# Kernel tuning notes

Hardware: AMD Instinct MI355X
Metric: run time of the kernel (lower is better)

Reference implementation:

```python
import jax, jax.numpy as jnp
import numpy as np

NHEADS = 16

def setup_inputs() -> dict:
    key = jax.random.key(0)
    ks = jax.random.split(key, 5)
    C = 1024
    d = C // NHEADS
    x  = jax.random.normal(ks[0], (2, 2048, C), dtype=jnp.float32)
    sc = 1.0 / np.sqrt(C)
    wq = jax.random.normal(ks[1], (C, C), dtype=jnp.float32) * sc
    wk = jax.random.normal(ks[2], (C, C), dtype=jnp.float32) * sc
    wv = jax.random.normal(ks[3], (C, C), dtype=jnp.float32) * sc
    wo = jax.random.normal(ks[4], (d, C), dtype=jnp.float32) * (1.0 / np.sqrt(d))
    return {"x": x, "wq": wq, "wk": wk, "wv": wv, "wo": wo}

def reference(x, wq, wk, wv, wo):
    B, T, C = x.shape
    H = NHEADS
    d = C // H

    def split_heads(y):
        return y.reshape(B, T, H, d).transpose(0, 2, 1, 3)  # [B,H,T,d]

    Q = split_heads(x @ wq)
    K = split_heads(x @ wk)
    V = split_heads(x @ wv)

    # scores[b,h,q,k]
    prod = jnp.einsum('bhqd,bhkd->bhqk', Q, K) / np.sqrt(d)

    # ALiBi bias: offset[h, q, k] = (k - q) * 2**(-8*(h+1)/H)
    idx = jnp.arange(T)
    slopes = jnp.exp2(-8.0 * (jnp.arange(H, dtype=jnp.float32) + 1.0) / H)
    bias = (idx[None, :] - idx[:, None]).astype(x.dtype) * slopes[:, None, None]
    prod = prod + bias[None]

    # causal tril mask: keep k <= q
    keep = idx[None, :] <= idx[:, None]  # [T_q, T_k]
    prod = jnp.where(keep[None, None], prod, -jnp.inf)

    # NOTE: original uses F.softmax(prod, 2) -> softmax over the QUERY axis.
    attention_weights = jax.nn.softmax(prod, axis=2)
    attention_output = jnp.einsum('bhqk,bhkd->bhqd', attention_weights, V)

    # per-head wo projection then sum over heads == (sum over heads) @ wo (linear)
    outputs = attention_output.sum(axis=1) @ wo  # [B,T,C]
    return x + outputs
```

## Files before the change

kernel.cpp:

```cpp
#include <hip/hip_runtime.h>
#include <math.h>

#define NB 2
#define NH 16
#define NT 2048
#define ND 64
#define NC 1024
#define L2E 1.44269504f

typedef __attribute__((ext_vector_type(4))) float f32x4;
typedef __attribute__((ext_vector_type(8))) short short8;
typedef __attribute__((ext_vector_type(4))) short short4_t;
typedef __attribute__((ext_vector_type(8))) unsigned short ushort8;
typedef __attribute__((ext_vector_type(4))) unsigned short ushort4_t;

__device__ const int WTAB[16] = {2,2,3,3,4,5,6,8,11,15,21,29,32,32,32,32};

#define GLOAD_LDS(gp, lp)                                                \
    __builtin_amdgcn_global_load_lds(                                    \
        (const __attribute__((address_space(1))) void*)(gp),             \
        (__attribute__((address_space(3))) void*)(lp), 16, 0, 0)

__device__ __forceinline__ int sigma_p(int p) {
    return 4 * ((p >> 3) & 3) + (p & 3) + 16 * ((p >> 2) & 1) + 32 * (p >> 5);
}

__device__ __forceinline__ unsigned short f2bf(float f) {
    unsigned u = __builtin_bit_cast(unsigned, f);
    unsigned r = (u + 0x7FFFu + ((u >> 16) & 1u)) >> 16;
    return (unsigned short)r;
}

__device__ __forceinline__ float bf2f(unsigned short s) {
    return __builtin_bit_cast(float, (unsigned)s << 16);
}

__device__ __forceinline__ unsigned cvtpk_bf16(float lo, float hi) {
    unsigned r;
    asm("v_cvt_pk_bf16_f32 %0, %1, %2" : "=v"(r) : "v"(lo), "v"(hi));
    return r;
}

__device__ __forceinline__ f32x4 mfma16(short8 a, short8 b, f32x4 c) {
    return __builtin_amdgcn_mfma_f32_16x16x32_bf16(a, b, c, 0, 0, 0);
}

__device__ __forceinline__ short8 frag_load(const unsigned short* rowp, int g, int half) {
    short8 v;
    short4_t lo = *(const short4_t*)(rowp + 4 * g + 32 * half);
    short4_t hi = *(const short4_t*)(rowp + 4 * g + 16 + 32 * half);
    #pragma unroll
    for (int j = 0; j < 4; ++j) { v[j] = lo[j]; v[4 + j] = hi[j]; }
    return v;
}

__device__ __forceinline__ short8 frag_g(const unsigned short* rowp, int g, int half) {
    return *(const short8*)(rowp + 8 * g + 32 * half);
}

__device__ __forceinline__ short8 frag_swz128(const unsigned short* tile, int row, int g, int half) {
    const char* p = (const char*)tile + row * 128 + (((g + 4 * half) ^ (row & 7)) << 4);
    return *(const short8*)p;
}

__device__ __forceinline__ short8 frag_swz32(const unsigned short* tile, int row, int g) {
    const char* p = (const char*)tile + row * 64 + (((g ^ ((row >> 1) & 3))) << 4);
    return *(const short8*)p;
}

__global__ __launch_bounds__(256) void cvt_x(const float* __restrict__ src,
                                             unsigned short* __restrict__ dst, int n4) {
    int i = blockIdx.x * 256 + threadIdx.x;
    if (i >= n4) return;
    const int blk = i >> 4, c4 = i & 15;
    const int gg = (c4 >> 1) & 3, bb = c4 & 1, hh = c4 >> 3;
    f32x4 v = ((const f32x4*)src)[blk * 16 + gg + 4 * bb + 8 * hh];
    ushort4_t o;
    #pragma unroll
    for (int j = 0; j < 4; ++j) o[j] = f2bf(v[j]);
    ((ushort4_t*)dst)[i] = o;
}

__global__ __launch_bounds__(256) void cvtW(const float* __restrict__ w0,
                                            const float* __restrict__ w1,
                                            const float* __restrict__ w2,
                                            const float* __restrict__ w3,
                                            unsigned short* __restrict__ Wt_all,
                                            unsigned short* __restrict__ Wot) {
    __shared__ __align__(16) float T[64][68];
    const int z = blockIdx.z;
    const int tid = threadIdx.x;
    if (z == 3) {
        if (blockIdx.x != 0) return;
        const int n0 = blockIdx.y * 64;
        #pragma unroll
        for (int p = 0; p < 4; ++p) {
            int r = 16 * p + (tid >> 4);
            int c = (tid & 15) * 4;
            *(f32x4*)&T[r][c] = *(const f32x4*)&w3[(size_t)r * NC + n0 + c];
        }
        __syncthreads();
        const int nr = tid >> 2, kc = (tid & 3) * 16;
        ushort8 o0, o1;
        #pragma unroll
        for (int j = 0; j < 8; ++j) { o0[j] = f2bf(T[kc + j][nr]); o1[j] = f2bf(T[kc + 8 + j][nr]); }
        unsigned short* q = Wot + (size_t)(n0 + nr) * ND + kc;
        *(ushort8*)q       = o0;
        *(ushort8*)(q + 8) = o1;
        return;
    }
    const float* W = (z == 0) ? w0 : ((z == 1) ? w1 : w2);
    unsigned short* Wt = Wt_all + (size_t)z * NC * NC;
    const int k0 = blockIdx.x * 64, n0 = blockIdx.y * 64;
    #pragma unroll
    for (int p = 0; p < 4; ++p) {
        int r = 16 * p + (tid >> 4);
        int c = (tid & 15) * 4;
        *(f32x4*)&T[r][c] = *(const f32x4*)&W[(size_t)(k0 + r) * NC + n0 + c];
    }
    __syncthreads();
    const int nr = tid >> 2, kc = (tid & 3) * 16;
    ushort8 o0, o1;
    #pragma unroll
    for (int j = 0; j < 8; ++j) o0[j] = f2bf(T[sigma_p(kc + j)][nr]);
    #pragma unroll
    for (int j = 0; j < 8; ++j) o1[j] = f2bf(T[sigma_p(kc + 8 + j)][nr]);
    unsigned short* q = Wt + (size_t)(n0 + nr) * NC + k0 + kc;
    *(ushort8*)q       = o0;
    *(ushort8*)(q + 8) = o1;
}

__global__ __launch_bounds__(256, 3) void gemm_qkv(const unsigned short* __restrict__ Xh,
                                                   const unsigned short* __restrict__ Wt_all,
                                                   unsigned short* __restrict__ qk_dst,
                                                   unsigned short* __restrict__ Vt) {
    __shared__ __align__(16) unsigned short Xs[3][4096];
    __shared__ __align__(16) unsigned short Ws[3][4096];
    const int tid = threadIdx.x;
    const int lane = tid & 63, w = tid >> 6;
    const int g = lane >> 4, l15 = lane & 15;
    const int wr = w >> 1, wc = w & 1;
    const int m0 = blockIdx.x * 128;
    const int which = blockIdx.y >> 3;
    const int n0 = (blockIdx.y & 7) * 128;
    const unsigned short* Wt = Wt_all + (size_t)which * NC * NC;

    const int sr[2] = { (0 * 256 + w * 64 + lane) >> 2, (1 * 256 + w * 64 + lane) >> 2 };
    const int sc[2] = { ((0 * 256 + w * 64 + lane) & 3) ^ ((sr[0] >> 1) & 3),
                        ((1 * 256 + w * 64 + lane) & 3) ^ ((sr[1] >> 1) & 3) };

    f32x4 acc[4][4] = {};

    auto stage = [&](int buf, int kt) {
        const size_t kb = (size_t)kt * 64;
        #pragma unroll
        for (int i = 0; i < 2; ++i) {
            const char* xs = (const char*)Xh + (size_t)(m0 + sr[i]) * 2048 + kb + (sc[i] << 4);
            GLOAD_LDS(xs, (char*)&Xs[buf][(i * 256 + w * 64) * 8]);
            const char* ws = (const char*)Wt + (size_t)(n0 + sr[i]) * 2048 + kb + (sc[i] << 4);
            GLOAD_LDS(ws, (char*)&Ws[buf][(i * 256 + w * 64) * 8]);
        }
    };

    stage(0, 0);
    stage(1, 1);
    int cur = 0, nxt = 2;

    for (int kt = 0; kt < 32; ++kt) {
        if (kt < 31) asm volatile("s_waitcnt vmcnt(4)" ::: "memory");
        else         asm volatile("s_waitcnt vmcnt(0)" ::: "memory");
        __builtin_amdgcn_s_barrier();
        if (kt + 2 < 32) stage(nxt, kt + 2);
        short8 a[4], b[4];
        #pragma unroll
        for (int mr = 0; mr < 4; ++mr)
            a[mr] = frag_swz32(Xs[cur], 64 * wr + 16 * mr + l15, g);
        #pragma unroll
        for (int nc = 0; nc < 4; ++nc)
            b[nc] = frag_swz32(Ws[cur], 64 * wc + 16 * nc + l15, g);
        __builtin_amdgcn_s_setprio(1);
        #pragma unroll
        for (int mr = 0; mr < 4; ++mr)
            #pragma unroll
            for (int nc = 0; nc < 4; ++nc)
                acc[mr][nc] = mfma16(a[mr], b[nc], acc[mr][nc]);
        __builtin_amdgcn_s_setprio(0);
        cur = (cur == 2) ? 0 : cur + 1;
        nxt = (nxt == 2) ? 0 : nxt + 1;
    }

    if (which < 2) {
        unsigned short* dst = qk_dst + (size_t)which * (NB * NH * NT * ND);
        #pragma unroll
        for (int mr = 0; mr < 4; ++mr) {
            #pragma unroll
            for (int nc = 0; nc < 4; ++nc) {
                const int n = n0 + 64 * wc + 16 * nc + l15;
                const int hh = n >> 6;
                const int dd = 32 * (nc >> 1) + 8 * (l15 >> 2) + 4 * (nc & 1) + (l15 & 3);
                #pragma unroll
                for (int r = 0; r < 4; ++r) {
                    const int m = m0 + 64 * wr + 16 * mr + 4 * g + r;
                    const int bb = m >> 11, tt = m & (NT - 1);
                    dst[(((size_t)bb * NH + hh) * NT + tt) * ND + dd] = f2bf(acc[mr][nc][r]);
                }
            }
        }
    } else {
        #pragma unroll
        for (int mr = 0; mr < 4; ++mr) {
            const int m = m0 + 64 * wr + 16 * mr + 4 * g;
            const int bb = m >> 11, tt = m & (NT - 1);
            const int tbase = (tt & ~63) + 32 * (mr >> 1) + 8 * g + 4 * (mr & 1);
            #pragma unroll
            for (int nc = 0; nc < 4; ++nc) {
                const int n = n0 + 64 * wc + 16 * nc + l15;
                const int hh = n >> 6, dd = n & 63;
                ushort4_t o;
                #pragma unroll
                for (int r = 0; r < 4; ++r) o[r] = f2bf(acc[mr][nc][r]);
                *(ushort4_t*)&Vt[(((size_t)bb * NH + hh) * ND + dd) * NT + tbase] = o;
            }
        }
    }
}

__global__ __launch_bounds__(256, 4) void colstats(const unsigned short* __restrict__ Qh,
                                                   const unsigned short* __restrict__ Kh,
                                                   unsigned short* __restrict__ Vt) {
    __shared__ __align__(16) unsigned short Qs[3][4096];
    __shared__ __align__(16) float Ssum[64];
    const int tid = threadIdx.x;
    const int lane = tid & 63, w = tid >> 6;
    const int g = lane >> 4, l15 = lane & 15;
    const int subrow = lane >> 3;
    const int src_off = (((lane & 7) ^ subrow) << 4);
    const int lin = blockIdx.x + 32 * blockIdx.y;
    const int xcd = lin & 7, idx = lin >> 3;
    const int slot = idx & 3;
    const int j = idx >> 2;
    const int hh = (slot & 1) ? (15 - xcd) : xcd;
    const int bh = ((slot >> 1) << 4) + hh;
    const float slL2 = exp2f(-0.5f * (float)(hh + 1)) * L2E;
    const float C1 = 0.125f * L2E;
    const float s16 = 16.f * slL2;
    const int Wt = WTAB[hh];
    const int qtend = min(32, j + Wt);

    const unsigned short* kr = Kh + ((size_t)bh * NT + 64 * j + 16 * w + l15) * ND;
    const short8 ak0 = frag_g(kr, g, 0), ak1 = frag_g(kr, g, 1);
    const int k0 = 64 * j + 16 * w + 4 * g;

    const char* Qbase = (const char*)(Qh + (size_t)bh * NT * ND);
    auto stage = [&](int buf, int qt) {
        const char* qs = Qbase + (size_t)(64 * qt + 16 * w + subrow) * 128 + src_off;
        char* qd = (char*)&Qs[buf][16 * w * 64];
        GLOAD_LDS(qs, qd);
        GLOAD_LDS(qs + 1024, qd + 1024);
    };

    f32x4 acc = {};
    float rs[4];
    #pragma unroll
    for (int r = 0; r < 4; ++r) rs[r] = (float)r * slL2;

    stage(0, j);
    if (j + 1 < qtend) stage(1, j + 1);
    int cur = 0, nxt = 2;

    for (int qt = j; qt < qtend; ++qt) {
        if (qt + 1 < qtend) asm volatile("s_waitcnt vmcnt(2)" ::: "memory");
        else                asm volatile("s_waitcnt vmcnt(0)" ::: "memory");
        __builtin_amdgcn_s_barrier();
        if (qt + 2 < qtend) stage(nxt, qt + 2);
        const unsigned short* tile = Qs[cur];
        short8 qf[8];
        #pragma unroll
        for (int q4 = 0; q4 < 4; ++q4) {
            qf[2 * q4]     = frag_swz128(tile, 16 * q4 + l15, g, 0);
            qf[2 * q4 + 1] = frag_swz128(tile, 16 * q4 + l15, g, 1);
        }
        float b0 = (float)(k0 - 64 * qt - l15) * slL2;
        const bool mask = (qt == j);
        #pragma unroll
        for (int q4 = 0; q4 < 4; ++q4) {
            f32x4 d = {};
            __builtin_amdgcn_s_setprio(1);
            d = mfma16(ak0, qf[2 * q4], d);
            d = mfma16(ak1, qf[2 * q4 + 1], d);
            __builtin_amdgcn_s_setprio(0);
            #pragma unroll
            for (int r = 0; r < 4; ++r) {
                float e = exp2f(fmaf(d[r], C1, b0 + rs[r]));
                if (mask && (16 * q4 + l15 < 16 * w + 4 * g + r)) e = 0.f;
                acc[r] += e;
            }
            b0 -= s16;
        }
        cur = (cur == 2) ? 0 : cur + 1;
        nxt = (nxt == 2) ? 0 : nxt + 1;
    }
    #pragma unroll
    for (int off = 1; off <= 8; off <<= 1)
        #pragma unroll
        for (int r = 0; r < 4; ++r) acc[r] += __shfl_xor(acc[r], off);
    if (l15 == 0) {
        #pragma unroll
        for (int r = 0; r < 4; ++r) Ssum[16 * w + 4 * g + r] = acc[r];
    }
    __syncthreads();

    unsigned short* Vst = Vt + (size_t)bh * ND * NT + 64 * j;
    #pragma unroll
    for (int it = 0; it < 4; ++it) {
        const int c = 256 * it + tid;
        const int d = c >> 4;
        const int tp4 = (c & 15) * 4;
        f32x4 s = *(const f32x4*)&Ssum[sigma_p(tp4)];
        unsigned short* p = Vst + (size_t)d * NT + tp4;
        ushort4_t v = *(const ushort4_t*)p;
        ushort4_t o;
        #pragma unroll
        for (int r = 0; r < 4; ++r) o[r] = f2bf(bf2f(v[r]) / s[r]);
        *(ushort4_t*)p = o;
    }
}

__global__ __launch_bounds__(256, 3) void attn_pv(const unsigned short* __restrict__ Qh,
                                                  const unsigned short* __restrict__ Kh,
                                                  const unsigned short* __restrict__ Vt,
                                                  unsigned short* __restrict__ att) {
    __shared__ __align__(16) unsigned short Ks[3][4096];
    __shared__ __align__(16) unsigned short Vs[3][4096];
    const int tid = threadIdx.x;
    const int lane = tid & 63, w = tid >> 6;
    const int g = lane >> 4, l15 = lane & 15;
    const int subrow = lane >> 3;
    const int src_off = (((lane & 7) ^ subrow) << 4);
    const int lin = blockIdx.x + 32 * blockIdx.y;
    const int xcd = lin & 7, idx = lin >> 3;
    const int slot = idx & 3;
    const int j = 31 - (idx >> 2);
    const int hh = (slot & 1) ? (15 - xcd) : xcd;
    const int bh = ((slot >> 1) << 4) + hh;
    const int bb = bh >> 4;
    const float slL2 = exp2f(-0.5f * (float)(hh + 1)) * L2E;
    const float C1 = 0.125f * L2E;
    const float s16 = 16.f * slL2;
    const int Wt = WTAB[hh];
    const int ktmin = max(0, j - Wt + 1);

    const int q = 64 * j + 16 * w + l15;
    short8 bq0, bq1;
    {
        const unsigned short* qr = Qh + ((size_t)bh * NT + q) * ND;
        bq0 = frag_g(qr, g, 0);
        bq1 = frag_g(qr, g, 1);
    }
    float rs[4];
    #pragma unroll
    for (int r = 0; r < 4; ++r) rs[r] = (float)r * slL2;

    auto stageKV = [&](int buf, int K0) {
        const char* ksrc = (const char*)Kh + (size_t)((size_t)bh * NT + K0 + 16 * w + subrow) * 128 + src_off;
        char* kdst = (char*)&Ks[buf][16 * w * 64];
        GLOAD_LDS(ksrc, kdst);
        GLOAD_LDS(ksrc + 1024, kdst + 1024);
        const char* vsrc = (const char*)Vt + ((((size_t)bh * ND + 16 * w + subrow) * NT + K0) << 1) + src_off;
        char* vdst = (char*)&Vs[buf][16 * w * 64];
        GLOAD_LDS(vsrc, vdst);
        GLOAD_LDS(vsrc + 8 * NT * 2, vdst + 1024);
    };

    stageKV(0, 64 * ktmin);
    if (ktmin < j) stageKV(1, 64 * (ktmin + 1));
    int cur = 0, nxt = 2;

    f32x4 o[4] = {};

    for (int kt = ktmin; kt <= j; ++kt) {
        if (kt < j) asm volatile("s_waitcnt vmcnt(4)" ::: "memory");
        else        asm volatile("s_waitcnt vmcnt(0)" ::: "memory");
        __builtin_amdgcn_s_barrier();
        if (kt + 2 <= j) stageKV(nxt, 64 * (kt + 2));
        const int K0 = 64 * kt;
        short8 kf[8], vf[8];
        #pragma unroll
        for (int s4 = 0; s4 < 4; ++s4) {
            kf[2 * s4]     = frag_swz128(Ks[cur], 16 * s4 + l15, g, 0);
            kf[2 * s4 + 1] = frag_swz128(Ks[cur], 16 * s4 + l15, g, 1);
            vf[2 * s4]     = frag_swz128(Vs[cur], 16 * s4 + l15, g, 0);
            vf[2 * s4 + 1] = frag_swz128(Vs[cur], 16 * s4 + l15, g, 1);
        }
        f32x4 pacc[4];
        __builtin_amdgcn_s_setprio(1);
        #pragma unroll
        for (int s4 = 0; s4 < 4; ++s4) {
            f32x4 d = {};
            d = mfma16(kf[2 * s4], bq0, d);
            d = mfma16(kf[2 * s4 + 1], bq1, d);
            pacc[s4] = d;
        }
        __builtin_amdgcn_s_setprio(0);
        union { unsigned u[4]; short8 s; } pa[2];
        float b = (float)(K0 + 4 * g - q) * slL2;
        const bool mask = (kt == j);
        #pragma unroll
        for (int s4 = 0; s4 < 4; ++s4) {
            float p[4];
            #pragma unroll
            for (int r = 0; r < 4; ++r)
                p[r] = exp2f(fmaf(pacc[s4][r], C1, b + rs[r]));
            if (mask) {
                #pragma unroll
                for (int r = 0; r < 4; ++r)
                    if (K0 + 16 * s4 + 4 * g + r > q) p[r] = 0.f;
            }
            pa[s4 >> 1].u[2 * (s4 & 1)]     = cvtpk_bf16(p[0], p[1]);
            pa[s4 >> 1].u[2 * (s4 & 1) + 1] = cvtpk_bf16(p[2], p[3]);
            b += s16;
        }
        __builtin_amdgcn_s_setprio(1);
        #pragma unroll
        for (int n = 0; n < 4; ++n) {
            o[n] = mfma16(pa[0].s, vf[2 * n], o[n]);
            o[n] = mfma16(pa[1].s, vf[2 * n + 1], o[n]);
        }
        __builtin_amdgcn_s_setprio(0);
        cur = (cur == 2) ? 0 : cur + 1;
        nxt = (nxt == 2) ? 0 : nxt + 1;
    }
    #pragma unroll
    for (int n = 0; n < 4; ++n) {
        #pragma unroll
        for (int r = 0; r < 4; ++r) {
            att[(((size_t)bb * NT + 64 * j + 16 * w + 4 * g + r) * NH + hh) * ND + 16 * n + l15] = f2bf(o[n][r]);
        }
    }
}

__global__ __launch_bounds__(256) void headsum(const unsigned short* __restrict__ att,
                                               unsigned short* __restrict__ A) {
    const int row = blockIdx.x * 16 + (threadIdx.x >> 4);
    const int d0 = (threadIdx.x & 15) * 4;
    const unsigned short* p = att + (size_t)row * (NH * ND) + d0;
    f32x4 s = {};
    #pragma unroll
    for (int h = 0; h < NH; ++h) {
        ushort4_t v = *(const ushort4_t*)(p + h * ND);
        #pragma unroll
        for (int jj = 0; jj < 4; ++jj) s[jj] += bf2f(v[jj]);
    }
    ushort4_t o;
    #pragma unroll
    for (int jj = 0; jj < 4; ++jj) o[jj] = f2bf(s[jj]);
    *(ushort4_t*)&A[(size_t)row * ND + d0] = o;
}

__global__ __launch_bounds__(256) void out_proj(const float* __restrict__ x,
                                                const unsigned short* __restrict__ A,
                                                const unsigned short* __restrict__ Wot,
                                                float* __restrict__ out) {
    const int tid = threadIdx.x;
    const int lane = tid & 63, w = tid >> 6;
    const int g = lane >> 4, l15 = lane & 15;
    const int m0 = blockIdx.x * 64, n0 = blockIdx.y * 64;

    const unsigned short* ar = A + (size_t)(m0 + 16 * w + l15) * ND;
    short8 a0 = frag_load(ar, g, 0);
    short8 a1 = frag_load(ar, g, 1);

    f32x4 acc[4] = {};
    #pragma unroll
    for (int ns = 0; ns < 4; ++ns) {
        const unsigned short* br = Wot + (size_t)(n0 + 16 * ns + l15) * ND;
        acc[ns] = mfma16(a0, frag_load(br, g, 0), acc[ns]);
        acc[ns] = mfma16(a1, frag_load(br, g, 1), acc[ns]);
    }
    #pragma unroll
    for (int ns = 0; ns < 4; ++ns) {
        #pragma unroll
        for (int r = 0; r < 4; ++r) {
            int m = m0 + 16 * w + 4 * g + r;
            int n = n0 + 16 * ns + l15;
            out[(size_t)m * NC + n] = x[(size_t)m * NC + n] + acc[ns][r];
        }
    }
}

extern "C" void kernel_launch(void* const* d_in, const int* in_sizes, int n_in,
                              void* d_out, int out_size, void* d_ws, size_t ws_size,
                              hipStream_t stream) {
    const float* x  = (const float*)d_in[0];
    const float* wq = (const float*)d_in[1];
    const float* wk = (const float*)d_in[2];
    const float* wv = (const float*)d_in[3];
    const float* wo = (const float*)d_in[4];
    float* out = (float*)d_out;

    const size_t MB = 1u << 20;
    const size_t KB = 1u << 10;
    unsigned char* w8 = (unsigned char*)d_ws;
    unsigned short* Xh  = (unsigned short*)(w8);
    unsigned short* Wta = (unsigned short*)(w8 + 8 * MB);
    unsigned short* Qh  = (unsigned short*)(w8 + 16 * MB);
    unsigned short* Kh  = (unsigned short*)(w8 + 24 * MB);
    unsigned short* Vt  = (unsigned short*)(w8 + 32 * MB);
    unsigned short* att = (unsigned short*)(w8 + 40 * MB);
    unsigned short* A   = (unsigned short*)(w8 + 48 * MB);
    unsigned short* Wot = (unsigned short*)(w8 + 48 * MB + 512 * KB);

    cvt_x<<<(NB * NT * NC) / 1024, 256, 0, stream>>>(x, Xh, (NB * NT * NC) / 4);
    cvtW<<<dim3(16, 16, 4), 256, 0, stream>>>(wq, wk, wv, wo, Wta, Wot);

    gemm_qkv<<<dim3(32, 24), 256, 0, stream>>>(Xh, Wta, Qh, Vt);

    colstats<<<dim3(32, 32), 256, 0, stream>>>(Qh, Kh, Vt);
    attn_pv<<<dim3(32, 32), 256, 0, stream>>>(Qh, Kh, Vt, att);

    headsum<<<(NB * NT) / 16, 256, 0, stream>>>(att, A);
    out_proj<<<dim3(64, 16), 256, 0, stream>>>(x, A, Wot, out);
}
```

Before: 127.1 us.

## Split colstats and attn_pv loops across two blocks by tile parity

Doubles the grid for the column-statistics and attention kernels. Each pair of blocks handles the even and odd tiles of the reduction loop. Partial column sums go to a two-slot buffer, and a new scale_v kernel combines them and normalizes V. Partial attention outputs go to two buffers that headsum adds together. This adds parallelism for long causal windows on lightly loaded heads, at the cost of an extra kernel launch, more workspace traffic, and an extra bf16 rounding of the partial outputs.

```diff
diff --git a/kernel.cpp b/kernel.cpp
--- a/kernel.cpp
+++ b/kernel.cpp
@@ -227,16 +227,17 @@
 
 __global__ __launch_bounds__(256, 4) void colstats(const unsigned short* __restrict__ Qh,
                                                    const unsigned short* __restrict__ Kh,
-                                                   unsigned short* __restrict__ Vt) {
+                                                   float* __restrict__ Lc2) {
     __shared__ __align__(16) unsigned short Qs[3][4096];
-    __shared__ __align__(16) float Ssum[64];
     const int tid = threadIdx.x;
     const int lane = tid & 63, w = tid >> 6;
     const int g = lane >> 4, l15 = lane & 15;
     const int subrow = lane >> 3;
     const int src_off = (((lane & 7) ^ subrow) << 4);
     const int lin = blockIdx.x + 32 * blockIdx.y;
-    const int xcd = lin & 7, idx = lin >> 3;
+    const int par = lin & 1;
+    const int rest = lin >> 1;
+    const int xcd = rest & 7, idx = rest >> 3;
     const int slot = idx & 3;
     const int j = idx >> 2;
     const int hh = (slot & 1) ? (15 - xcd) : xcd;
@@ -246,6 +247,7 @@
     const float s16 = 16.f * slL2;
     const int Wt = WTAB[hh];
     const int qtend = min(32, j + Wt);
+    const int qt0 = j + ((par ^ j) & 1);
 
     const unsigned short* kr = Kh + ((size_t)bh * NT + 64 * j + 16 * w + l15) * ND;
     const short8 ak0 = frag_g(kr, g, 0), ak1 = frag_g(kr, g, 1);
@@ -264,15 +266,15 @@
     #pragma unroll
     for (int r = 0; r < 4; ++r) rs[r] = (float)r * slL2;
 
-    stage(0, j);
-    if (j + 1 < qtend) stage(1, j + 1);
+    if (qt0 < qtend) stage(0, qt0);
+    if (qt0 + 2 < qtend) stage(1, qt0 + 2);
     int cur = 0, nxt = 2;
 
-    for (int qt = j; qt < qtend; ++qt) {
-        if (qt + 1 < qtend) asm volatile("s_waitcnt vmcnt(2)" ::: "memory");
+    for (int qt = qt0; qt < qtend; qt += 2) {
+        if (qt + 2 < qtend) asm volatile("s_waitcnt vmcnt(2)" ::: "memory");
         else                asm volatile("s_waitcnt vmcnt(0)" ::: "memory");
         __builtin_amdgcn_s_barrier();
-        if (qt + 2 < qtend) stage(nxt, qt + 2);
+        if (qt + 4 < qtend) stage(nxt, qt + 4);
         const unsigned short* tile = Qs[cur];
         short8 qf[8];
         #pragma unroll
@@ -305,31 +307,33 @@
         #pragma unroll
         for (int r = 0; r < 4; ++r) acc[r] += __shfl_xor(acc[r], off);
     if (l15 == 0) {
-        #pragma unroll
-        for (int r = 0; r < 4; ++r) Ssum[16 * w + 4 * g + r] = acc[r];
-    }
-    __syncthreads();
-
-    unsigned short* Vst = Vt + (size_t)bh * ND * NT + 64 * j;
-    #pragma unroll
-    for (int it = 0; it < 4; ++it) {
-        const int c = 256 * it + tid;
-        const int d = c >> 4;
-        const int tp4 = (c & 15) * 4;
-        f32x4 s = *(const f32x4*)&Ssum[sigma_p(tp4)];
-        unsigned short* p = Vst + (size_t)d * NT + tp4;
-        ushort4_t v = *(const ushort4_t*)p;
-        ushort4_t o;
-        #pragma unroll
-        for (int r = 0; r < 4; ++r) o[r] = f2bf(bf2f(v[r]) / s[r]);
-        *(ushort4_t*)p = o;
-    }
+        float* Lp = Lc2 + (size_t)(par * 32 + bh) * NT;
+        #pragma unroll
+        for (int r = 0; r < 4; ++r) Lp[k0 + r] = acc[r];
+    }
+}
+
+__global__ __launch_bounds__(256) void scale_v(const float* __restrict__ Lc2,
+                                               unsigned short* __restrict__ Vt) {
+    const int i = blockIdx.x * 256 + threadIdx.x;
+    const int bh = i >> 15;
+    const int tpos4 = (i & 511) * 4;
+    const int tlog = (tpos4 & ~63) + sigma_p(tpos4 & 63);
+    f32x4 a = *(const f32x4*)(Lc2 + (size_t)bh * NT + tlog);
+    f32x4 b = *(const f32x4*)(Lc2 + (size_t)(32 + bh) * NT + tlog);
+    ushort4_t v = ((const ushort4_t*)Vt)[i];
+    ushort4_t o;
+    #pragma unroll
+    for (int j = 0; j < 4; ++j)
+        o[j] = f2bf(bf2f(v[j]) / (a[j] + b[j]));
+    ((ushort4_t*)Vt)[i] = o;
 }
 
 __global__ __launch_bounds__(256, 3) void attn_pv(const unsigned short* __restrict__ Qh,
                                                   const unsigned short* __restrict__ Kh,
                                                   const unsigned short* __restrict__ Vt,
-                                                  unsigned short* __restrict__ att) {
+                                                  unsigned short* __restrict__ att,
+                                                  unsigned short* __restrict__ att2) {
     __shared__ __align__(16) unsigned short Ks[3][4096];
     __shared__ __align__(16) unsigned short Vs[3][4096];
     const int tid = threadIdx.x;
@@ -338,7 +342,9 @@
     const int subrow = lane >> 3;
     const int src_off = (((lane & 7) ^ subrow) << 4);
     const int lin = blockIdx.x + 32 * blockIdx.y;
-    const int xcd = lin & 7, idx = lin >> 3;
+    const int par = lin & 1;
+    const int rest = lin >> 1;
+    const int xcd = rest & 7, idx = rest >> 3;
     const int slot = idx & 3;
     const int j = 31 - (idx >> 2);
     const int hh = (slot & 1) ? (15 - xcd) : xcd;
@@ -349,6 +355,7 @@
     const float s16 = 16.f * slL2;
     const int Wt = WTAB[hh];
     const int ktmin = max(0, j - Wt + 1);
+    const int kt0 = ktmin + ((par ^ ktmin) & 1);
 
     const int q = 64 * j + 16 * w + l15;
     short8 bq0, bq1;
@@ -372,17 +379,17 @@
         GLOAD_LDS(vsrc + 8 * NT * 2, vdst + 1024);
     };
 
-    stageKV(0, 64 * ktmin);
-    if (ktmin < j) stageKV(1, 64 * (ktmin + 1));
+    if (kt0 <= j) stageKV(0, 64 * kt0);
+    if (kt0 + 2 <= j) stageKV(1, 64 * (kt0 + 2));
     int cur = 0, nxt = 2;
 
     f32x4 o[4] = {};
 
-    for (int kt = ktmin; kt <= j; ++kt) {
-        if (kt < j) asm volatile("s_waitcnt vmcnt(4)" ::: "memory");
-        else        asm volatile("s_waitcnt vmcnt(0)" ::: "memory");
+    for (int kt = kt0; kt <= j; kt += 2) {
+        if (kt + 2 <= j) asm volatile("s_waitcnt vmcnt(4)" ::: "memory");
+        else             asm volatile("s_waitcnt vmcnt(0)" ::: "memory");
         __builtin_amdgcn_s_barrier();
-        if (kt + 2 <= j) stageKV(nxt, 64 * (kt + 2));
+        if (kt + 4 <= j) stageKV(nxt, 64 * (kt + 4));
         const int K0 = 64 * kt;
         short8 kf[8], vf[8];
         #pragma unroll
@@ -430,26 +437,30 @@
         cur = (cur == 2) ? 0 : cur + 1;
         nxt = (nxt == 2) ? 0 : nxt + 1;
     }
+    unsigned short* dst = (par == 0) ? att : att2;
     #pragma unroll
     for (int n = 0; n < 4; ++n) {
         #pragma unroll
         for (int r = 0; r < 4; ++r) {
-            att[(((size_t)bb * NT + 64 * j + 16 * w + 4 * g + r) * NH + hh) * ND + 16 * n + l15] = f2bf(o[n][r]);
+            dst[(((size_t)bb * NT + 64 * j + 16 * w + 4 * g + r) * NH + hh) * ND + 16 * n + l15] = f2bf(o[n][r]);
         }
     }
 }
 
 __global__ __launch_bounds__(256) void headsum(const unsigned short* __restrict__ att,
+                                               const unsigned short* __restrict__ att2,
                                                unsigned short* __restrict__ A) {
     const int row = blockIdx.x * 16 + (threadIdx.x >> 4);
     const int d0 = (threadIdx.x & 15) * 4;
-    const unsigned short* p = att + (size_t)row * (NH * ND) + d0;
+    const unsigned short* p  = att  + (size_t)row * (NH * ND) + d0;
+    const unsigned short* p2 = att2 + (size_t)row * (NH * ND) + d0;
     f32x4 s = {};
     #pragma unroll
     for (int h = 0; h < NH; ++h) {
-        ushort4_t v = *(const ushort4_t*)(p + h * ND);
-        #pragma unroll
-        for (int jj = 0; jj < 4; ++jj) s[jj] += bf2f(v[jj]);
+        ushort4_t v  = *(const ushort4_t*)(p + h * ND);
+        ushort4_t v2 = *(const ushort4_t*)(p2 + h * ND);
+        #pragma unroll
+        for (int jj = 0; jj < 4; ++jj) s[jj] += bf2f(v[jj]) + bf2f(v2[jj]);
     }
     ushort4_t o;
     #pragma unroll
@@ -501,23 +512,26 @@
     const size_t MB = 1u << 20;
     const size_t KB = 1u << 10;
     unsigned char* w8 = (unsigned char*)d_ws;
-    unsigned short* Xh  = (unsigned short*)(w8);
-    unsigned short* Wta = (unsigned short*)(w8 + 8 * MB);
-    unsigned short* Qh  = (unsigned short*)(w8 + 16 * MB);
-    unsigned short* Kh  = (unsigned short*)(w8 + 24 * MB);
-    unsigned short* Vt  = (unsigned short*)(w8 + 32 * MB);
-    unsigned short* att = (unsigned short*)(w8 + 40 * MB);
-    unsigned short* A   = (unsigned short*)(w8 + 48 * MB);
-    unsigned short* Wot = (unsigned short*)(w8 + 48 * MB + 512 * KB);
+    unsigned short* Xh   = (unsigned short*)(w8);
+    unsigned short* Wta  = (unsigned short*)(w8 + 8 * MB);
+    unsigned short* Qh   = (unsigned short*)(w8 + 16 * MB);
+    unsigned short* Kh   = (unsigned short*)(w8 + 24 * MB);
+    unsigned short* Vt   = (unsigned short*)(w8 + 32 * MB);
+    unsigned short* att  = (unsigned short*)(w8 + 40 * MB);
+    unsigned short* att2 = (unsigned short*)(w8 + 48 * MB);
+    float*          Lc2  = (float*)(w8 + 56 * MB);
+    unsigned short* A    = (unsigned short*)(w8 + 56 * MB + 512 * KB);
+    unsigned short* Wot  = (unsigned short*)(w8 + 57 * MB);
 
     cvt_x<<<(NB * NT * NC) / 1024, 256, 0, stream>>>(x, Xh, (NB * NT * NC) / 4);
     cvtW<<<dim3(16, 16, 4), 256, 0, stream>>>(wq, wk, wv, wo, Wta, Wot);
 
     gemm_qkv<<<dim3(32, 24), 256, 0, stream>>>(Xh, Wta, Qh, Vt);
 
-    colstats<<<dim3(32, 32), 256, 0, stream>>>(Qh, Kh, Vt);
-    attn_pv<<<dim3(32, 32), 256, 0, stream>>>(Qh, Kh, Vt, att);
-
-    headsum<<<(NB * NT) / 16, 256, 0, stream>>>(att, A);
+    colstats<<<dim3(32, 64), 256, 0, stream>>>(Qh, Kh, Lc2);
+    scale_v<<<(32 * ND * NT / 4) / 256, 256, 0, stream>>>(Lc2, Vt);
+    attn_pv<<<dim3(32, 64), 256, 0, stream>>>(Qh, Kh, Vt, att, att2);
+
+    headsum<<<(NB * NT) / 16, 256, 0, stream>>>(att, att2, A);
     out_proj<<<dim3(64, 16), 256, 0, stream>>>(x, A, Wot, out);
 }
```

Result: slower. 129.7 us (+2.0%).

## Split long-window heads across two blocks to balance attention workload

Applied to the files above, without the earlier changes.

Heads 10-15 have the widest ALiBi key windows, so their attention blocks run much longer than the rest. Each such (batch, head, query tile) is now split into two blocks, each covering half the key tiles. The second half writes to a separate att2 buffer that headsum adds in. The grid grows from 1024 to 1408 blocks and the XCD-aware head mapping is replaced, trading extra partial-output traffic and a larger headsum read for better load balance.

```diff
diff --git a/kernel.cpp b/kernel.cpp
--- a/kernel.cpp
+++ b/kernel.cpp
@@ -329,7 +329,8 @@
 __global__ __launch_bounds__(256, 3) void attn_pv(const unsigned short* __restrict__ Qh,
                                                   const unsigned short* __restrict__ Kh,
                                                   const unsigned short* __restrict__ Vt,
-                                                  unsigned short* __restrict__ att) {
+                                                  unsigned short* __restrict__ att,
+                                                  unsigned short* __restrict__ att2) {
     __shared__ __align__(16) unsigned short Ks[3][4096];
     __shared__ __align__(16) unsigned short Vs[3][4096];
     const int tid = threadIdx.x;
@@ -338,17 +339,40 @@
     const int subrow = lane >> 3;
     const int src_off = (((lane & 7) ^ subrow) << 4);
     const int lin = blockIdx.x + 32 * blockIdx.y;
-    const int xcd = lin & 7, idx = lin >> 3;
-    const int slot = idx & 3;
-    const int j = 31 - (idx >> 2);
-    const int hh = (slot & 1) ? (15 - xcd) : xcd;
-    const int bh = ((slot >> 1) << 4) + hh;
+
+    int j, hh, bh, half;
+    if (lin < 768) {
+        half = (lin < 384) ? 1 : 0;
+        const int v = (lin < 384) ? lin : (lin - 384);
+        j = 31 - (v / 12);
+        const int r = v % 12;
+        hh = 10 + (r % 6);
+        bh = (r / 6) * 16 + hh;
+    } else {
+        half = -1;
+        const int v = lin - 768;
+        j = 31 - (v / 20);
+        const int r = v % 20;
+        hh = r % 10;
+        bh = (r / 10) * 16 + hh;
+    }
     const int bb = bh >> 4;
     const float slL2 = exp2f(-0.5f * (float)(hh + 1)) * L2E;
     const float C1 = 0.125f * L2E;
     const float s16 = 16.f * slL2;
     const int Wt = WTAB[hh];
     const int ktmin = max(0, j - Wt + 1);
+
+    int ktA, ktB;
+    unsigned short* dst;
+    if (half < 0) {
+        ktA = ktmin; ktB = j; dst = att;
+    } else {
+        const int range = j - ktmin + 1;
+        const int nlow = (range + 1) >> 1;
+        if (half == 0) { ktA = ktmin;        ktB = ktmin + nlow - 1; dst = att; }
+        else           { ktA = ktmin + nlow; ktB = j;                dst = att2; }
+    }
 
     const int q = 64 * j + 16 * w + l15;
     short8 bq0, bq1;
@@ -372,82 +396,92 @@
         GLOAD_LDS(vsrc + 8 * NT * 2, vdst + 1024);
     };
 
-    stageKV(0, 64 * ktmin);
-    if (ktmin < j) stageKV(1, 64 * (ktmin + 1));
-    int cur = 0, nxt = 2;
-
     f32x4 o[4] = {};
 
-    for (int kt = ktmin; kt <= j; ++kt) {
-        if (kt < j) asm volatile("s_waitcnt vmcnt(4)" ::: "memory");
-        else        asm volatile("s_waitcnt vmcnt(0)" ::: "memory");
-        __builtin_amdgcn_s_barrier();
-        if (kt + 2 <= j) stageKV(nxt, 64 * (kt + 2));
-        const int K0 = 64 * kt;
-        short8 kf[8], vf[8];
-        #pragma unroll
-        for (int s4 = 0; s4 < 4; ++s4) {
-            kf[2 * s4]     = frag_swz128(Ks[cur], 16 * s4 + l15, g, 0);
-            kf[2 * s4 + 1] = frag_swz128(Ks[cur], 16 * s4 + l15, g, 1);
-            vf[2 * s4]     = frag_swz128(Vs[cur], 16 * s4 + l15, g, 0);
-            vf[2 * s4 + 1] = frag_swz128(Vs[cur], 16 * s4 + l15, g, 1);
-        }
-        f32x4 pacc[4];
-        __builtin_amdgcn_s_setprio(1);
-        #pragma unroll
-        for (int s4 = 0; s4 < 4; ++s4) {
-            f32x4 d = {};
-            d = mfma16(kf[2 * s4], bq0, d);
-            d = mfma16(kf[2 * s4 + 1], bq1, d);
-            pacc[s4] = d;
-        }
-        __builtin_amdgcn_s_setprio(0);
-        union { unsigned u[4]; short8 s; } pa[2];
-        float b = (float)(K0 + 4 * g - q) * slL2;
-        const bool mask = (kt == j);
-        #pragma unroll
-        for (int s4 = 0; s4 < 4; ++s4) {
-            float p[4];
-            #pragma unroll
-            for (int r = 0; r < 4; ++r)
-                p[r] = exp2f(fmaf(pacc[s4][r], C1, b + rs[r]));
-            if (mask) {
+    if (ktA <= ktB) {
+        stageKV(0, 64 * ktA);
+        if (ktA < ktB) stageKV(1, 64 * (ktA + 1));
+        int cur = 0, nxt = 2;
+
+        for (int kt = ktA; kt <= ktB; ++kt) {
+            if (kt < ktB) asm volatile("s_waitcnt vmcnt(4)" ::: "memory");
+            else          asm volatile("s_waitcnt vmcnt(0)" ::: "memory");
+            __builtin_amdgcn_s_barrier();
+            if (kt + 2 <= ktB) stageKV(nxt, 64 * (kt + 2));
+            const int K0 = 64 * kt;
+            short8 kf[8], vf[8];
+            #pragma unroll
+            for (int s4 = 0; s4 < 4; ++s4) {
+                kf[2 * s4]     = frag_swz128(Ks[cur], 16 * s4 + l15, g, 0);
+                kf[2 * s4 + 1] = frag_swz128(Ks[cur], 16 * s4 + l15, g, 1);
+                vf[2 * s4]     = frag_swz128(Vs[cur], 16 * s4 + l15, g, 0);
+                vf[2 * s4 + 1] = frag_swz128(Vs[cur], 16 * s4 + l15, g, 1);
+            }
+            f32x4 pacc[4];
+            __builtin_amdgcn_s_setprio(1);
+            #pragma unroll
+            for (int s4 = 0; s4 < 4; ++s4) {
+                f32x4 d = {};
+                d = mfma16(kf[2 * s4], bq0, d);
+                d = mfma16(kf[2 * s4 + 1], bq1, d);
+                pacc[s4] = d;
+            }
+            __builtin_amdgcn_s_setprio(0);
+            union { unsigned u[4]; short8 s; } pa[2];
+            float b = (float)(K0 + 4 * g - q) * slL2;
+            const bool mask = (kt == j);
+            #pragma unroll
+            for (int s4 = 0; s4 < 4; ++s4) {
+                float p[4];
                 #pragma unroll
                 for (int r = 0; r < 4; ++r)
-                    if (K0 + 16 * s4 + 4 * g + r > q) p[r] = 0.f;
-            }
-            pa[s4 >> 1].u[2 * (s4 & 1)]     = cvtpk_bf16(p[0], p[1]);
-            pa[s4 >> 1].u[2 * (s4 & 1) + 1] = cvtpk_bf16(p[2], p[3]);
-            b += s16;
-        }
-        __builtin_amdgcn_s_setprio(1);
-        #pragma unroll
-        for (int n = 0; n < 4; ++n) {
-            o[n] = mfma16(pa[0].s, vf[2 * n], o[n]);
-            o[n] = mfma16(pa[1].s, vf[2 * n + 1], o[n]);
-        }
-        __builtin_amdgcn_s_setprio(0);
-        cur = (cur == 2) ? 0 : cur + 1;
-        nxt = (nxt == 2) ? 0 : nxt + 1;
+                    p[r] = exp2f(fmaf(pacc[s4][r], C1, b + rs[r]));
+                if (mask) {
+                    #pragma unroll
+                    for (int r = 0; r < 4; ++r)
+                        if (K0 + 16 * s4 + 4 * g + r > q) p[r] = 0.f;
+                }
+                pa[s4 >> 1].u[2 * (s4 & 1)]     = cvtpk_bf16(p[0], p[1]);
+                pa[s4 >> 1].u[2 * (s4 & 1) + 1] = cvtpk_bf16(p[2], p[3]);
+                b += s16;
+            }
+            __builtin_amdgcn_s_setprio(1);
+            #pragma unroll
+            for (int n = 0; n < 4; ++n) {
+                o[n] = mfma16(pa[0].s, vf[2 * n], o[n]);
+                o[n] = mfma16(pa[1].s, vf[2 * n + 1], o[n]);
+            }
+            __builtin_amdgcn_s_setprio(0);
+            cur = (cur == 2) ? 0 : cur + 1;
+            nxt = (nxt == 2) ? 0 : nxt + 1;
+        }
     }
     #pragma unroll
     for (int n = 0; n < 4; ++n) {
         #pragma unroll
         for (int r = 0; r < 4; ++r) {
-            att[(((size_t)bb * NT + 64 * j + 16 * w + 4 * g + r) * NH + hh) * ND + 16 * n + l15] = f2bf(o[n][r]);
+            dst[(((size_t)bb * NT + 64 * j + 16 * w + 4 * g + r) * NH + hh) * ND + 16 * n + l15] = f2bf(o[n][r]);
         }
     }
 }
 
 __global__ __launch_bounds__(256) void headsum(const unsigned short* __restrict__ att,
+                                               const unsigned short* __restrict__ att2,
                                                unsigned short* __restrict__ A) {
     const int row = blockIdx.x * 16 + (threadIdx.x >> 4);
     const int d0 = (threadIdx.x & 15) * 4;
-    const unsigned short* p = att + (size_t)row * (NH * ND) + d0;
+    const unsigned short* p  = att  + (size_t)row * (NH * ND) + d0;
+    const unsigned short* p2 = att2 + (size_t)row * (NH * ND) + d0;
     f32x4 s = {};
     #pragma unroll
     for (int h = 0; h < NH; ++h) {
         ushort4_t v = *(const ushort4_t*)(p + h * ND);
+        #pragma unroll
+        for (int jj = 0; jj < 4; ++jj) s[jj] += bf2f(v[jj]);
+    }
+    #pragma unroll
+    for (int h = 10; h < NH; ++h) {
+        ushort4_t v = *(const ushort4_t*)(p2 + h * ND);
         #pragma unroll
         for (int jj = 0; jj < 4; ++jj) s[jj] += bf2f(v[jj]);
     }
@@ -501,14 +535,15 @@
     const size_t MB = 1u << 20;
     const size_t KB = 1u << 10;
     unsigned char* w8 = (unsigned char*)d_ws;
-    unsigned short* Xh  = (unsigned short*)(w8);
-    unsigned short* Wta = (unsigned short*)(w8 + 8 * MB);
-    unsigned short* Qh  = (unsigned short*)(w8 + 16 * MB);
-    unsigned short* Kh  = (unsigned short*)(w8 + 24 * MB);
-    unsigned short* Vt  = (unsigned short*)(w8 + 32 * MB);
-    unsigned short* att = (unsigned short*)(w8 + 40 * MB);
-    unsigned short* A   = (unsigned short*)(w8 + 48 * MB);
-    unsigned short* Wot = (unsigned short*)(w8 + 48 * MB + 512 * KB);
+    unsigned short* Xh   = (unsigned short*)(w8);
+    unsigned short* Wta  = (unsigned short*)(w8 + 8 * MB);
+    unsigned short* Qh   = (unsigned short*)(w8 + 16 * MB);
+    unsigned short* Kh   = (unsigned short*)(w8 + 24 * MB);
+    unsigned short* Vt   = (unsigned short*)(w8 + 32 * MB);
+    unsigned short* att  = (unsigned short*)(w8 + 40 * MB);
+    unsigned short* att2 = (unsigned short*)(w8 + 48 * MB);
+    unsigned short* A    = (unsigned short*)(w8 + 56 * MB);
+    unsigned short* Wot  = (unsigned short*)(w8 + 56 * MB + 512 * KB);
 
     cvt_x<<<(NB * NT * NC) / 1024, 256, 0, stream>>>(x, Xh, (NB * NT * NC) / 4);
     cvtW<<<dim3(16, 16, 4), 256, 0, stream>>>(wq, wk, wv, wo, Wta, Wot);
@@ -516,8 +551,8 @@
     gemm_qkv<<<dim3(32, 24), 256, 0, stream>>>(Xh, Wta, Qh, Vt);
 
     colstats<<<dim3(32, 32), 256, 0, stream>>>(Qh, Kh, Vt);
-    attn_pv<<<dim3(32, 32), 256, 0, stream>>>(Qh, Kh, Vt, att);
-
-    headsum<<<(NB * NT) / 16, 256, 0, stream>>>(att, A);
+    attn_pv<<<dim3(32, 44), 256, 0, stream>>>(Qh, Kh, Vt, att, att2);
+
+    headsum<<<(NB * NT) / 16, 256, 0, stream>>>(att, att2, A);
     out_proj<<<dim3(64, 16), 256, 0, stream>>>(x, A, Wot, out);
 }
```

Result: no change. 125.6 us (-1.2%).
